# Kernel optimization log

Hardware: AMD Instinct MI355X
Metric: run time of the kernel (lower is better)

Reference implementation:

```python
import jax, jax.numpy as jnp
import numpy as np

B, N, E, H, SD, HID = 4, 512, 1024, 16, 64, 64
D = E // H  # head_dim


def setup_inputs() -> dict:
    key = jax.random.key(0)
    ks = jax.random.split(key, 20)
    s = lambda i, shape, scale: (jax.random.normal(ks[i], shape, dtype=jnp.float32) * scale)
    inp = {
        "query": s(0, (B, N, E), 1.0),
        "key": s(1, (B, N, E), 1.0),
        "value": s(2, (B, N, E), 1.0),
        "state_embeddings": s(3, (B, N, SD), 1.0),
        # projection weights stored [in, out] (transposed vs torch nn.Linear)
        "Wq": s(4, (E, E), E ** -0.5), "bq": jnp.zeros((E,), jnp.float32),
        "Wk": s(5, (E, E), E ** -0.5), "bk": jnp.zeros((E,), jnp.float32),
        "Wv": s(6, (E, E), E ** -0.5), "bv": jnp.zeros((E,), jnp.float32),
        "Wo": s(7, (E, E), E ** -0.5), "bo": jnp.zeros((E,), jnp.float32),
        # CAB compatibility MLP: Linear(2*SD->HID), ReLU, Linear(HID->HID), ReLU, Linear(HID->H)
        "W1": s(8, (2 * SD, HID), (2 * SD) ** -0.5), "b1": jnp.zeros((HID,), jnp.float32),
        "W2": s(9, (HID, HID), HID ** -0.5), "b2": jnp.zeros((HID,), jnp.float32),
        "W3": s(10, (HID, H), HID ** -0.5), "b3": jnp.zeros((H,), jnp.float32),
        "head_temps": jnp.ones((H,), jnp.float32),
    }
    return inp


def reference(query, key, value, state_embeddings,
              Wq, bq, Wk, bk, Wv, bv, Wo, bo,
              W1, b1, W2, b2, W3, b3, head_temps):
    scale = D ** -0.5
    q = (query @ Wq + bq).reshape(B, N, H, D)
    k = (key @ Wk + bk).reshape(B, N, H, D)
    v = (value @ Wv + bv).reshape(B, N, H, D)
    # [B, H, T, S]
    scores = jnp.einsum("bthd,bshd->bhts", q, k) * scale

    # CAB bias: MLP([e_i; e_j]) -> split first layer to avoid materializing pairs
    hi = state_embeddings @ W1[:SD]          # [B, N, HID]
    hj = state_embeddings @ W1[SD:]          # [B, N, HID]
    h = jax.nn.relu(hi[:, :, None, :] + hj[:, None, :, :] + b1)  # [B, N, N, HID]
    h = jax.nn.relu(h @ W2 + b2)
    comp = h @ W3 + b3                        # [B, N, N, H]
    bias = jnp.transpose(comp, (0, 3, 1, 2)) * head_temps[None, :, None, None]
    scores = scores + bias

    attn = jax.nn.softmax(scores, axis=-1)
    out = jnp.einsum("bhts,bshd->bthd", attn, v).reshape(B, N, E)
    return out @ Wo + bo
```

## Files before the change

### kernel.cpp

```cpp
#include <hip/hip_runtime.h>
#include <hip/hip_bf16.h>

typedef unsigned short u16;
typedef short short8 __attribute__((ext_vector_type(8)));
typedef float f32x4 __attribute__((ext_vector_type(4)));
typedef unsigned short u16x4 __attribute__((ext_vector_type(4)));

#define BB 4
#define NS 512
#define EE 1024
#define HH 16
#define DD 64
#define MM (BB*NS)
#define NSQ 2
#define SQW (NS/NSQ)

__device__ __forceinline__ u16 f2bfh(float x) {
  __hip_bfloat16 h = __float2bfloat16(x);
  union { __hip_bfloat16 h; u16 u; } c; c.h = h; return c.u;
}
__device__ __forceinline__ unsigned pkbf(float a, float b) {
  union { __hip_bfloat16 h; u16 u; } ca, cb;
  ca.h = __float2bfloat16(a); cb.h = __float2bfloat16(b);
  return (unsigned)ca.u | ((unsigned)cb.u << 16);
}
union S8 { short8 s; unsigned u[4]; };

__device__ __forceinline__ void gload_lds16(const void* g, void* l) {
  __builtin_amdgcn_global_load_lds(
      (const __attribute__((address_space(1))) unsigned int*)g,
      (__attribute__((address_space(3))) unsigned int*)l, 16, 0, 0);
}


__global__ void cvt_inputs(const float* __restrict__ q, const float* __restrict__ k,
                           const float* __restrict__ v,
                           u16* __restrict__ qb, u16* __restrict__ kb, u16* __restrict__ vb) {
  size_t g = (size_t)blockIdx.x * 256 + threadIdx.x;
  size_t e = g << 3;
  int seg = (int)(e >> 21);
  size_t off = e & ((1u << 21) - 1);
  const float* src = seg == 0 ? q : (seg == 1 ? k : v);
  u16* dst = seg == 0 ? qb : (seg == 1 ? kb : vb);
  float4 f0 = *(const float4*)(src + off);
  float4 f1 = *(const float4*)(src + off + 4);
  S8 r;
  r.u[0] = pkbf(f0.x, f0.y); r.u[1] = pkbf(f0.z, f0.w);
  r.u[2] = pkbf(f1.x, f1.y); r.u[3] = pkbf(f1.z, f1.w);
  *(short8*)(dst + off) = r.s;
}

__global__ void cvt_w(const float* __restrict__ Wq, const float* __restrict__ Wk,
                      const float* __restrict__ Wv, const float* __restrict__ Wo,
                      u16* __restrict__ WqT, u16* __restrict__ WkT,
                      u16* __restrict__ WvT, u16* __restrict__ WoT) {
  int z = blockIdx.z;
  const float* W = z == 0 ? Wq : z == 1 ? Wk : z == 2 ? Wv : Wo;
  u16* WT = z == 0 ? WqT : z == 1 ? WkT : z == 2 ? WvT : WoT;
  int n0 = blockIdx.x << 5, k0 = blockIdx.y << 5;
  __shared__ float tile[32][33];
  int tx = threadIdx.x & 31, ty = threadIdx.x >> 5;
  #pragma unroll
  for (int i = 0; i < 4; ++i) {
    int r = (i << 3) + ty;
    tile[r][tx] = W[(size_t)(k0 + r) * EE + n0 + tx];
  }
  __syncthreads();
  #pragma unroll
  for (int i = 0; i < 4; ++i) {
    int r = (i << 3) + ty;
    WT[(size_t)(n0 + r) * EE + k0 + tx] = f2bfh(tile[tx][r]);
  }
}

__global__ void cvt_w_small(const float* __restrict__ W2, const float* __restrict__ W3,
                            u16* __restrict__ W2T, u16* __restrict__ W3P) {
  int tid = threadIdx.x;
  for (int i = tid; i < 4096; i += 256) {
    int n = i >> 6, k = i & 63;
    W2T[i] = f2bfh(W2[k * 64 + n]);
  }
  for (int i = tid; i < 1024; i += 256) {
    int h = i >> 6, rem = i & 63;
    int k2 = rem >> 5, gg = (rem >> 3) & 3, j = rem & 7;
    int c = (2 * k2 + (j >> 2)) * 16 + gg * 4 + (j & 3);
    W3P[i] = f2bfh(W3[c * 16 + h]);
  }
}


__global__ void hi_hj_kernel(const float* __restrict__ se, const float* __restrict__ W1,
                             const float* __restrict__ b1,
                             float* __restrict__ hi, float* __restrict__ hj) {
  int tid = threadIdx.x;
  int row = blockIdx.x * 4 + (tid >> 6);
  int c = tid & 63;
  float ah = b1[c], aj = 0.f;
  #pragma unroll 8
  for (int k = 0; k < 64; ++k) {
    float s = se[row * 64 + k];
    ah += s * W1[k * 64 + c];
    aj += s * W1[(k + 64) * 64 + c];
  }
  hi[row * 64 + c] = ah;
  hj[row * 64 + c] = aj;
}


template <int MODE>
__device__ __forceinline__ void gemm_body(const u16* __restrict__ A, const u16* __restrict__ Bt,
                                          const float* __restrict__ bias, void* __restrict__ Cout) {
  __shared__ u16 As[128 * 32];
  __shared__ u16 Bs[128 * 32];
  const int tid = threadIdx.x, lane = tid & 63, wave = tid >> 6;
  const int m0 = blockIdx.x * 128, n0 = blockIdx.y * 128;
  const int wr = wave >> 1, wc = wave & 1;

  const f32x4 zero = {0.f, 0.f, 0.f, 0.f};
  f32x4 acc[4][4];
  #pragma unroll
  for (int i = 0; i < 4; ++i)
    #pragma unroll
    for (int j = 0; j < 4; ++j) acc[i][j] = zero;

  const int rA = lane >> 2;
  const int cA = (lane & 3) << 3;

  for (int kt = 0; kt < EE; kt += 32) {
    #pragma unroll
    for (int i = 0; i < 2; ++i) {
      int base = ((i << 2) + wave) << 9;
      int row = (base >> 5) + rA;
      gload_lds16(A  + (size_t)(m0 + row) * EE + kt + cA, As + base);
      gload_lds16(Bt + (size_t)(n0 + row) * EE + kt + cA, Bs + base);
    }
    __syncthreads();
    short8 af[4], bfr[4];
    #pragma unroll
    for (int mf = 0; mf < 4; ++mf) {
      int row = wr * 64 + mf * 16 + (lane & 15);
      af[mf] = *(const short8*)(As + row * 32 + ((lane >> 4) << 3));
    }
    #pragma unroll
    for (int nf = 0; nf < 4; ++nf) {
      int row = wc * 64 + nf * 16 + (lane & 15);
      bfr[nf] = *(const short8*)(Bs + row * 32 + ((lane >> 4) << 3));
    }
    #pragma unroll
    for (int mf = 0; mf < 4; ++mf)
      #pragma unroll
      for (int nf = 0; nf < 4; ++nf)
        acc[mf][nf] = __builtin_amdgcn_mfma_f32_16x16x32_bf16(af[mf], bfr[nf], acc[mf][nf], 0, 0, 0);
    __syncthreads();
  }

  #pragma unroll
  for (int mf = 0; mf < 4; ++mf) {
    #pragma unroll
    for (int nf = 0; nf < 4; ++nf) {
      int col = n0 + wc * 64 + nf * 16 + (lane & 15);
      float bv = bias[col];
      #pragma unroll
      for (int j = 0; j < 4; ++j) {
        int rowm = m0 + wr * 64 + mf * 16 + ((lane >> 4) << 2) + j;
        float v = acc[mf][nf][j] + bv;
        if (MODE == 2) {
          ((float*)Cout)[(size_t)rowm * EE + col] = v;
        } else {
          int bb = rowm >> 9, r = rowm & 511;
          int h = col >> 6, d = col & 63;
          size_t off;
          if (MODE == 0)
            off = ((((size_t)bb * HH + h) * 32 + (r >> 4)) << 10) + ((size_t)(d >> 5) << 9)
                + ((size_t)((((d >> 3) & 3) << 4) + (r & 15)) << 3) + (d & 7);
          else
            off = (((((size_t)bb * HH + h) * 16 + (r >> 5)) * 4 + (d >> 4)) << 9)
                + ((size_t)((((r >> 3) & 3) << 4) + (d & 15)) << 3) + (r & 7);
          ((u16*)Cout)[off] = f2bfh(v);
        }
      }
    }
  }
}

__global__ __launch_bounds__(256, 2) void gemm_proj(
    const u16* __restrict__ qb, const u16* __restrict__ kb, const u16* __restrict__ vb,
    const u16* __restrict__ WqT, const u16* __restrict__ WkT, const u16* __restrict__ WvT,
    const float* __restrict__ bq, const float* __restrict__ bk, const float* __restrict__ bv_,
    u16* __restrict__ qF, u16* __restrict__ kF, u16* __restrict__ vF) {
  int z = blockIdx.z;
  if (z == 0)      gemm_body<0>(qb, WqT, bq, qF);
  else if (z == 1) gemm_body<0>(kb, WkT, bk, kF);
  else             gemm_body<1>(vb, WvT, bv_, vF);
}

__global__ __launch_bounds__(256, 2) void gemm_final(
    const u16* __restrict__ A, const u16* __restrict__ WoT,
    const float* __restrict__ bo, float* __restrict__ C) {
  gemm_body<2>(A, WoT, bo, C);
}


__global__ __launch_bounds__(512, 2) void fused_cab_attn(
    const float* __restrict__ hi, const float* __restrict__ hj,
    const u16* __restrict__ W2T, const u16* __restrict__ W3P,
    const float* __restrict__ b2, const float* __restrict__ b3,
    const float* __restrict__ temps,
    const u16* __restrict__ qF, const u16* __restrict__ kF,
    const u16* __restrict__ vF,
    float* __restrict__ Opart, float* __restrict__ mlpart) {
  const int b = blockIdx.x >> 1, sq = blockIdx.x & 1, tt = blockIdx.y;
  const int t0 = tt << 4;
  const int tid = threadIdx.x, lane = tid & 63, wave = tid >> 6;
  const int g = lane >> 4, sl = lane & 15;

  __shared__ float hi_s[16][80];
  __shared__ float hj_s[32][65];
  __shared__ float b2_s[64], b3_s[16], tp_s[16];
  __shared__ float comp3[16 * 273];
  __shared__ u16 Pl[8][16][40];

  if (tid < 256) {
    int r = tid >> 4, c4 = (tid & 15) << 2;
    float4 hv = *(const float4*)(hi + ((size_t)(b * NS + t0 + r) << 6) + c4);
    *(f32x4*)&hi_s[r][c4] = (f32x4){hv.x, hv.y, hv.z, hv.w};
  } else {
    int ix = tid - 256;
    if (ix < 64) b2_s[ix] = b2[ix];
    else if (ix < 80) b3_s[ix - 64] = b3[ix - 64];
    else if (ix < 96) tp_s[ix - 80] = temps[ix - 80];
  }

  const f32x4 zero = {0.f, 0.f, 0.f, 0.f};
  f32x4 acc[2][4];
  #pragma unroll
  for (int i = 0; i < 2; ++i)
    #pragma unroll
    for (int j = 0; j < 4; ++j) acc[i][j] = zero;
  float m_run[2] = {-3e38f, -3e38f};
  float l_run[2] = {0.f, 0.f};

  for (int pr = 0; pr < 8; ++pr) {
    const int s0p = sq * SQW + (pr << 5);
    __syncthreads();
    {
      int r = tid >> 4, c4 = (tid & 15) << 2;
      float4 a = *(const float4*)(hj + ((size_t)(b * NS + s0p + r) << 6) + c4);
      hj_s[r][c4 + 0] = a.x; hj_s[r][c4 + 1] = a.y;
      hj_s[r][c4 + 2] = a.z; hj_s[r][c4 + 3] = a.w;
    }

    float vsc[2][2][4];

    #pragma unroll
    for (int ta = 0; ta < 2; ++ta) {
      __syncthreads();
      {
        float hjv[2][8];
        #pragma unroll
        for (int kk = 0; kk < 2; ++kk)
          #pragma unroll
          for (int j = 0; j < 8; ++j)
            hjv[kk][j] = hj_s[(ta << 4) + sl][kk * 32 + (g << 3) + j];

        short8 w3f[2];
        #pragma unroll
        for (int k2 = 0; k2 < 2; ++k2)
          w3f[k2] = *(const short8*)(W3P + (sl << 6) + k2 * 32 + (g << 3));

        float b2v[4][4];
        #pragma unroll
        for (int mfc = 0; mfc < 4; ++mfc)
          #pragma unroll
          for (int jj = 0; jj < 4; ++jj)
            b2v[mfc][jj] = b2_s[mfc * 16 + (g << 2) + jj];

        #pragma unroll
        for (int q = 0; q < 2; ++q) {
          int tl = (wave << 1) + q;
          short8 xb[2];
          #pragma unroll
          for (int kk = 0; kk < 2; ++kk) {
            int c0 = kk * 32 + (g << 3);
            f32x4 h0 = *(const f32x4*)&hi_s[tl][c0];
            f32x4 h1 = *(const f32x4*)&hi_s[tl][c0 + 4];
            float x[8];
            #pragma unroll
            for (int j = 0; j < 4; ++j) {
              x[j]     = fmaxf(h0[j] + hjv[kk][j], 0.f);
              x[j + 4] = fmaxf(h1[j] + hjv[kk][j + 4], 0.f);
            }
            S8 r;
            r.u[0] = pkbf(x[0], x[1]); r.u[1] = pkbf(x[2], x[3]);
            r.u[2] = pkbf(x[4], x[5]); r.u[3] = pkbf(x[6], x[7]);
            xb[kk] = r.s;
          }
          f32x4 accY[4];
          #pragma unroll
          for (int i = 0; i < 4; ++i) accY[i] = zero;
          #pragma unroll
          for (int kk = 0; kk < 2; ++kk)
            #pragma unroll
            for (int mfc = 0; mfc < 4; ++mfc) {
              short8 w2 = *(const short8*)(W2T + ((mfc * 16 + sl) << 6) + kk * 32 + (g << 3));
              accY[mfc] = __builtin_amdgcn_mfma_f32_16x16x32_bf16(w2, xb[kk], accY[mfc], 0, 0, 0);
            }
          f32x4 compD = zero;
          #pragma unroll
          for (int k2 = 0; k2 < 2; ++k2) {
            float y[8];
            #pragma unroll
            for (int j = 0; j < 4; ++j) {
              y[j]     = fmaxf(accY[2 * k2][j]     + b2v[2 * k2][j],     0.f);
              y[j + 4] = fmaxf(accY[2 * k2 + 1][j] + b2v[2 * k2 + 1][j], 0.f);
            }
            S8 r;
            r.u[0] = pkbf(y[0], y[1]); r.u[1] = pkbf(y[2], y[3]);
            r.u[2] = pkbf(y[4], y[5]); r.u[3] = pkbf(y[6], y[7]);
            compD = __builtin_amdgcn_mfma_f32_16x16x32_bf16(w3f[k2], r.s, compD, 0, 0, 0);
          }
          #pragma unroll
          for (int jj = 0; jj < 4; ++jj) {
            int h = (g << 2) + jj;
            comp3[h * 273 + sl * 17 + tl] = (compD[jj] + b3_s[h]) * tp_s[h];
          }
        }
      }
      __syncthreads();
      const int s16 = (sq << 4) + (pr << 1) + ta;
      #pragma unroll
      for (int hh = 0; hh < 2; ++hh) {
        int h = (wave << 1) + hh;
        const u16* qb_ = qF + ((((size_t)b * HH + h) * 32 + tt) << 10) + (lane << 3);
        const u16* kb_ = kF + ((((size_t)b * HH + h) * 32 + s16) << 10) + (lane << 3);
        f32x4 accS = zero;
        accS = __builtin_amdgcn_mfma_f32_16x16x32_bf16(*(const short8*)kb_, *(const short8*)qb_, accS, 0, 0, 0);
        accS = __builtin_amdgcn_mfma_f32_16x16x32_bf16(*(const short8*)(kb_ + 512), *(const short8*)(qb_ + 512), accS, 0, 0, 0);
        #pragma unroll
        for (int j = 0; j < 4; ++j)
          vsc[ta][hh][j] = accS[j] * 0.125f + comp3[h * 273 + ((g << 2) + j) * 17 + sl];
      }
    }

    #pragma unroll
    for (int hh = 0; hh < 2; ++hh) {
      int h = (wave << 1) + hh;
      float e[8];
      float mx = -3e38f;
      #pragma unroll
      for (int j = 0; j < 4; ++j)
        mx = fmaxf(mx, fmaxf(vsc[0][hh][j], vsc[1][hh][j]));
      mx = fmaxf(mx, __shfl_xor(mx, 16, 64));
      mx = fmaxf(mx, __shfl_xor(mx, 32, 64));
      float mnew = fmaxf(m_run[hh], mx);
      float c = __expf(m_run[hh] - mnew);
      m_run[hh] = mnew;
      #pragma unroll
      for (int ta = 0; ta < 2; ++ta)
        #pragma unroll
        for (int j = 0; j < 4; ++j)
          e[ta * 4 + j] = __expf(vsc[ta][hh][j] - mnew);
      float ps = ((e[0] + e[1]) + (e[2] + e[3])) + ((e[4] + e[5]) + (e[6] + e[7]));
      ps += __shfl_xor(ps, 16, 64);
      ps += __shfl_xor(ps, 32, 64);
      l_run[hh] = l_run[hh] * c + ps;

      uint2 wA; wA.x = pkbf(e[0], e[1]); wA.y = pkbf(e[2], e[3]);
      uint2 wB; wB.x = pkbf(e[4], e[5]); wB.y = pkbf(e[6], e[7]);
      *(uint2*)&Pl[wave][sl][(g << 2)]      = wA;
      *(uint2*)&Pl[wave][sl][16 + (g << 2)] = wB;
      short8 pf = *(const short8*)&Pl[wave][sl][(g << 3)];

      float cb[4];
      #pragma unroll
      for (int j = 0; j < 4; ++j) cb[j] = __shfl(c, (g << 2) + j, 64);

      const u16* vb0 = vF + (((((size_t)b * HH + h) * 16 + (sq << 3) + pr) * 4) << 9) + (lane << 3);
      #pragma unroll
      for (int nf = 0; nf < 4; ++nf) {
        #pragma unroll
        for (int j = 0; j < 4; ++j) acc[hh][nf][j] *= cb[j];
        short8 vv = *(const short8*)(vb0 + ((size_t)nf << 9));
        acc[hh][nf] = __builtin_amdgcn_mfma_f32_16x16x32_bf16(pf, vv, acc[hh][nf], 0, 0, 0);
      }
    }
  }

  size_t obase = ((size_t)sq * MM + (size_t)b * NS + t0) * EE;
  #pragma unroll
  for (int hh = 0; hh < 2; ++hh) {
    int h = (wave << 1) + hh;
    #pragma unroll
    for (int nf = 0; nf < 4; ++nf)
      #pragma unroll
      for (int j = 0; j < 4; ++j)
        Opart[obase + (size_t)((g << 2) + j) * EE + (h << 6) + nf * 16 + sl] = acc[hh][nf][j];
  }
  if (g == 0) {
    #pragma unroll
    for (int hh = 0; hh < 2; ++hh) {
      int h = (wave << 1) + hh;
      size_t mlb = (((size_t)sq * MM + b * NS + t0 + sl) * HH + h) * 2;
      mlpart[mlb] = m_run[hh];
      mlpart[mlb + 1] = l_run[hh];
    }
  }
}


__global__ void combine_pv(const float* __restrict__ Opart, const float* __restrict__ mlpart,
                           u16* __restrict__ attn_out) {
  int row = blockIdx.x;
  int tid = threadIdx.x;
  int c4 = tid << 2;
  int h = c4 >> 6;
  float m[NSQ], l[NSQ];
  #pragma unroll
  for (int pq = 0; pq < NSQ; ++pq) {
    size_t mb = (((size_t)pq * MM + row) * HH + h) * 2;
    m[pq] = mlpart[mb]; l[pq] = mlpart[mb + 1];
  }
  float M = m[0];
  #pragma unroll
  for (int pq = 1; pq < NSQ; ++pq) M = fmaxf(M, m[pq]);
  float den = 0.f;
  f32x4 num = {0.f, 0.f, 0.f, 0.f};
  #pragma unroll
  for (int pq = 0; pq < NSQ; ++pq) {
    float w = __expf(m[pq] - M);
    den += w * l[pq];
    f32x4 o = *(const f32x4*)(Opart + ((size_t)pq * MM + row) * EE + c4);
    #pragma unroll
    for (int i = 0; i < 4; ++i) num[i] += w * o[i];
  }
  float r = 1.0f / den;
  u16x4 out;
  #pragma unroll
  for (int i = 0; i < 4; ++i) out[i] = f2bfh(num[i] * r);
  *(u16x4*)(attn_out + (size_t)row * EE + c4) = out;
}


extern "C" void kernel_launch(void* const* d_in, const int* in_sizes, int n_in,
                              void* d_out, int out_size, void* d_ws, size_t ws_size,
                              hipStream_t stream) {
  const float* query = (const float*)d_in[0];
  const float* key   = (const float*)d_in[1];
  const float* value = (const float*)d_in[2];
  const float* se    = (const float*)d_in[3];
  const float* Wq = (const float*)d_in[4];  const float* bq = (const float*)d_in[5];
  const float* Wk = (const float*)d_in[6];  const float* bk = (const float*)d_in[7];
  const float* Wv = (const float*)d_in[8];  const float* bv = (const float*)d_in[9];
  const float* Wo = (const float*)d_in[10]; const float* bo = (const float*)d_in[11];
  const float* W1 = (const float*)d_in[12]; const float* b1 = (const float*)d_in[13];
  const float* W2 = (const float*)d_in[14]; const float* b2 = (const float*)d_in[15];
  const float* W3 = (const float*)d_in[16]; const float* b3 = (const float*)d_in[17];
  const float* temps = (const float*)d_in[18];

  char* p = (char*)d_ws;
  auto alloc = [&](size_t bytes) { char* r = p; p += (bytes + 255) & ~(size_t)255; return r; };
  u16* qb  = (u16*)alloc((size_t)MM * EE * 2);
  u16* kb  = (u16*)alloc((size_t)MM * EE * 2);
  u16* vb  = (u16*)alloc((size_t)MM * EE * 2);
  u16* WqT = (u16*)alloc((size_t)EE * EE * 2);
  u16* WkT = (u16*)alloc((size_t)EE * EE * 2);
  u16* WvT = (u16*)alloc((size_t)EE * EE * 2);
  u16* WoT = (u16*)alloc((size_t)EE * EE * 2);
  u16* W2T = (u16*)alloc(4096 * 2);
  u16* W3P = (u16*)alloc(1024 * 2);
  u16* qF  = (u16*)alloc((size_t)MM * EE * 2);
  u16* kF  = (u16*)alloc((size_t)MM * EE * 2);
  u16* vF  = (u16*)alloc((size_t)MM * EE * 2);
  float* hi = (float*)alloc((size_t)MM * 64 * 4);
  float* hj = (float*)alloc((size_t)MM * 64 * 4);
  float* Opart = (float*)alloc((size_t)NSQ * MM * EE * 4);
  float* mlpart = (float*)alloc((size_t)NSQ * MM * HH * 2 * 4);
  u16* attn_out = (u16*)alloc((size_t)MM * EE * 2);
  (void)ws_size; (void)in_sizes; (void)n_in; (void)out_size;

  cvt_inputs<<<3072, 256, 0, stream>>>(query, key, value, qb, kb, vb);
  cvt_w<<<dim3(32, 32, 4), 256, 0, stream>>>(Wq, Wk, Wv, Wo, WqT, WkT, WvT, WoT);
  cvt_w_small<<<1, 256, 0, stream>>>(W2, W3, W2T, W3P);
  hi_hj_kernel<<<512, 256, 0, stream>>>(se, W1, b1, hi, hj);
  gemm_proj<<<dim3(16, 8, 3), 256, 0, stream>>>(qb, kb, vb, WqT, WkT, WvT, bq, bk, bv, qF, kF, vF);
  fused_cab_attn<<<dim3(8, 32, 1), 512, 0, stream>>>(hi, hj, W2T, W3P, b2, b3, temps,
                                                     qF, kF, vF, Opart, mlpart);
  combine_pv<<<MM, 256, 0, stream>>>(Opart, mlpart, attn_out);
  gemm_final<<<dim3(16, 8, 1), 256, 0, stream>>>(attn_out, WoT, bo, (float*)d_out);
}
```

Before: 122.7 us.

## Split attention key range four ways and hoist per-block constants out of loop

Increases the key-range split from 2 to 4, doubling the grid of the fused CAB+attention kernel to 512 blocks for better CU occupancy. Moves W3, b2, b3, temps and Q fragments into registers loaded once per block instead of per iteration. Double-buffers comp3 so both 16-key sub-tiles are computed before one barrier, cutting syncs per iteration. The trade-offs are more register pressure, larger partial output buffers, and more work for the combine kernel. The combine kernel (not shown) must handle NSQ=4 through the macro.

```diff
diff --git a/kernel.cpp b/kernel.cpp
--- a/kernel.cpp
+++ b/kernel.cpp
@@ -12,7 +12,7 @@
 #define HH 16
 #define DD 64
 #define MM (BB*NS)
-#define NSQ 2
+#define NSQ 4
 #define SQW (NS/NSQ)
 
 __device__ __forceinline__ u16 f2bfh(float x) {
@@ -209,26 +209,48 @@
     const u16* __restrict__ qF, const u16* __restrict__ kF,
     const u16* __restrict__ vF,
     float* __restrict__ Opart, float* __restrict__ mlpart) {
-  const int b = blockIdx.x >> 1, sq = blockIdx.x & 1, tt = blockIdx.y;
+  const int b = blockIdx.x >> 2, sq = blockIdx.x & 3, tt = blockIdx.y;
   const int t0 = tt << 4;
   const int tid = threadIdx.x, lane = tid & 63, wave = tid >> 6;
   const int g = lane >> 4, sl = lane & 15;
 
   __shared__ float hi_s[16][80];
   __shared__ float hj_s[32][65];
-  __shared__ float b2_s[64], b3_s[16], tp_s[16];
-  __shared__ float comp3[16 * 273];
+  __shared__ float comp3[2][16 * 273];
   __shared__ u16 Pl[8][16][40];
 
   if (tid < 256) {
     int r = tid >> 4, c4 = (tid & 15) << 2;
     float4 hv = *(const float4*)(hi + ((size_t)(b * NS + t0 + r) << 6) + c4);
     *(f32x4*)&hi_s[r][c4] = (f32x4){hv.x, hv.y, hv.z, hv.w};
-  } else {
-    int ix = tid - 256;
-    if (ix < 64) b2_s[ix] = b2[ix];
-    else if (ix < 80) b3_s[ix - 64] = b3[ix - 64];
-    else if (ix < 96) tp_s[ix - 80] = temps[ix - 80];
+  }
+
+  short8 w3f[2];
+  #pragma unroll
+  for (int k2 = 0; k2 < 2; ++k2)
+    w3f[k2] = *(const short8*)(W3P + (sl << 6) + k2 * 32 + (g << 3));
+
+  float b2v[4][4];
+  #pragma unroll
+  for (int mfc = 0; mfc < 4; ++mfc)
+    #pragma unroll
+    for (int jj = 0; jj < 4; ++jj)
+      b2v[mfc][jj] = b2[mfc * 16 + (g << 2) + jj];
+
+  float b3v[4], tpv[4];
+  #pragma unroll
+  for (int jj = 0; jj < 4; ++jj) {
+    b3v[jj] = b3[(g << 2) + jj];
+    tpv[jj] = temps[(g << 2) + jj];
+  }
+
+  short8 qf[2][2];
+  #pragma unroll
+  for (int hh = 0; hh < 2; ++hh) {
+    int h = (wave << 1) + hh;
+    const u16* qb_ = qF + ((((size_t)b * HH + h) * 32 + tt) << 10) + (lane << 3);
+    qf[hh][0] = *(const short8*)qb_;
+    qf[hh][1] = *(const short8*)(qb_ + 512);
   }
 
   const f32x4 zero = {0.f, 0.f, 0.f, 0.f};
@@ -240,7 +262,7 @@
   float m_run[2] = {-3e38f, -3e38f};
   float l_run[2] = {0.f, 0.f};
 
-  for (int pr = 0; pr < 8; ++pr) {
+  for (int pr = 0; pr < NSQ; ++pr) {
     const int s0p = sq * SQW + (pr << 5);
     __syncthreads();
     {
@@ -249,96 +271,84 @@
       hj_s[r][c4 + 0] = a.x; hj_s[r][c4 + 1] = a.y;
       hj_s[r][c4 + 2] = a.z; hj_s[r][c4 + 3] = a.w;
     }
-
-    float vsc[2][2][4];
+    __syncthreads();
 
     #pragma unroll
     for (int ta = 0; ta < 2; ++ta) {
-      __syncthreads();
-      {
-        float hjv[2][8];
+      float hjv[2][8];
+      #pragma unroll
+      for (int kk = 0; kk < 2; ++kk)
+        #pragma unroll
+        for (int j = 0; j < 8; ++j)
+          hjv[kk][j] = hj_s[(ta << 4) + sl][kk * 32 + (g << 3) + j];
+
+      #pragma unroll
+      for (int q = 0; q < 2; ++q) {
+        int tl = (wave << 1) + q;
+        short8 xb[2];
+        #pragma unroll
+        for (int kk = 0; kk < 2; ++kk) {
+          int c0 = kk * 32 + (g << 3);
+          f32x4 h0 = *(const f32x4*)&hi_s[tl][c0];
+          f32x4 h1 = *(const f32x4*)&hi_s[tl][c0 + 4];
+          float x[8];
+          #pragma unroll
+          for (int j = 0; j < 4; ++j) {
+            x[j]     = fmaxf(h0[j] + hjv[kk][j], 0.f);
+            x[j + 4] = fmaxf(h1[j] + hjv[kk][j + 4], 0.f);
+          }
+          S8 r;
+          r.u[0] = pkbf(x[0], x[1]); r.u[1] = pkbf(x[2], x[3]);
+          r.u[2] = pkbf(x[4], x[5]); r.u[3] = pkbf(x[6], x[7]);
+          xb[kk] = r.s;
+        }
+        f32x4 accY[4];
+        #pragma unroll
+        for (int i = 0; i < 4; ++i) accY[i] = zero;
         #pragma unroll
         for (int kk = 0; kk < 2; ++kk)
           #pragma unroll
-          for (int j = 0; j < 8; ++j)
-            hjv[kk][j] = hj_s[(ta << 4) + sl][kk * 32 + (g << 3) + j];
-
-        short8 w3f[2];
-        #pragma unroll
-        for (int k2 = 0; k2 < 2; ++k2)
-          w3f[k2] = *(const short8*)(W3P + (sl << 6) + k2 * 32 + (g << 3));
-
-        float b2v[4][4];
-        #pragma unroll
-        for (int mfc = 0; mfc < 4; ++mfc)
+          for (int mfc = 0; mfc < 4; ++mfc) {
+            short8 w2 = *(const short8*)(W2T + ((mfc * 16 + sl) << 6) + kk * 32 + (g << 3));
+            accY[mfc] = __builtin_amdgcn_mfma_f32_16x16x32_bf16(w2, xb[kk], accY[mfc], 0, 0, 0);
+          }
+        f32x4 compD = zero;
+        #pragma unroll
+        for (int k2 = 0; k2 < 2; ++k2) {
+          float y[8];
           #pragma unroll
-          for (int jj = 0; jj < 4; ++jj)
-            b2v[mfc][jj] = b2_s[mfc * 16 + (g << 2) + jj];
-
-        #pragma unroll
-        for (int q = 0; q < 2; ++q) {
-          int tl = (wave << 1) + q;
-          short8 xb[2];
-          #pragma unroll
-          for (int kk = 0; kk < 2; ++kk) {
-            int c0 = kk * 32 + (g << 3);
-            f32x4 h0 = *(const f32x4*)&hi_s[tl][c0];
-            f32x4 h1 = *(const f32x4*)&hi_s[tl][c0 + 4];
-            float x[8];
-            #pragma unroll
-            for (int j = 0; j < 4; ++j) {
-              x[j]     = fmaxf(h0[j] + hjv[kk][j], 0.f);
-              x[j + 4] = fmaxf(h1[j] + hjv[kk][j + 4], 0.f);
-            }
-            S8 r;
-            r.u[0] = pkbf(x[0], x[1]); r.u[1] = pkbf(x[2], x[3]);
-            r.u[2] = pkbf(x[4], x[5]); r.u[3] = pkbf(x[6], x[7]);
-            xb[kk] = r.s;
+          for (int j = 0; j < 4; ++j) {
+            y[j]     = fmaxf(accY[2 * k2][j]     + b2v[2 * k2][j],     0.f);
+            y[j + 4] = fmaxf(accY[2 * k2 + 1][j] + b2v[2 * k2 + 1][j], 0.f);
           }
-          f32x4 accY[4];
-          #pragma unroll
-          for (int i = 0; i < 4; ++i) accY[i] = zero;
-          #pragma unroll
-          for (int kk = 0; kk < 2; ++kk)
-            #pragma unroll
-            for (int mfc = 0; mfc < 4; ++mfc) {
-              short8 w2 = *(const short8*)(W2T + ((mfc * 16 + sl) << 6) + kk * 32 + (g << 3));
-              accY[mfc] = __builtin_amdgcn_mfma_f32_16x16x32_bf16(w2, xb[kk], accY[mfc], 0, 0, 0);
-            }
-          f32x4 compD = zero;
-          #pragma unroll
-          for (int k2 = 0; k2 < 2; ++k2) {
-            float y[8];
-            #pragma unroll
-            for (int j = 0; j < 4; ++j) {
-              y[j]     = fmaxf(accY[2 * k2][j]     + b2v[2 * k2][j],     0.f);
-              y[j + 4] = fmaxf(accY[2 * k2 + 1][j] + b2v[2 * k2 + 1][j], 0.f);
-            }
-            S8 r;
-            r.u[0] = pkbf(y[0], y[1]); r.u[1] = pkbf(y[2], y[3]);
-            r.u[2] = pkbf(y[4], y[5]); r.u[3] = pkbf(y[6], y[7]);
-            compD = __builtin_amdgcn_mfma_f32_16x16x32_bf16(w3f[k2], r.s, compD, 0, 0, 0);
-          }
-          #pragma unroll
-          for (int jj = 0; jj < 4; ++jj) {
-            int h = (g << 2) + jj;
-            comp3[h * 273 + sl * 17 + tl] = (compD[jj] + b3_s[h]) * tp_s[h];
-          }
+          S8 r;
+          r.u[0] = pkbf(y[0], y[1]); r.u[1] = pkbf(y[2], y[3]);
+          r.u[2] = pkbf(y[4], y[5]); r.u[3] = pkbf(y[6], y[7]);
+          compD = __builtin_amdgcn_mfma_f32_16x16x32_bf16(w3f[k2], r.s, compD, 0, 0, 0);
+        }
+        #pragma unroll
+        for (int jj = 0; jj < 4; ++jj) {
+          int h = (g << 2) + jj;
+          comp3[ta][h * 273 + sl * 17 + tl] = (compD[jj] + b3v[jj]) * tpv[jj];
         }
       }
-      __syncthreads();
-      const int s16 = (sq << 4) + (pr << 1) + ta;
+    }
+    __syncthreads();
+
+    float vsc[2][2][4];
+    #pragma unroll
+    for (int ta = 0; ta < 2; ++ta) {
+      const int s16 = (sq << 3) + (pr << 1) + ta;
       #pragma unroll
       for (int hh = 0; hh < 2; ++hh) {
         int h = (wave << 1) + hh;
-        const u16* qb_ = qF + ((((size_t)b * HH + h) * 32 + tt) << 10) + (lane << 3);
         const u16* kb_ = kF + ((((size_t)b * HH + h) * 32 + s16) << 10) + (lane << 3);
         f32x4 accS = zero;
-        accS = __builtin_amdgcn_mfma_f32_16x16x32_bf16(*(const short8*)kb_, *(const short8*)qb_, accS, 0, 0, 0);
-        accS = __builtin_amdgcn_mfma_f32_16x16x32_bf16(*(const short8*)(kb_ + 512), *(const short8*)(qb_ + 512), accS, 0, 0, 0);
+        accS = __builtin_amdgcn_mfma_f32_16x16x32_bf16(*(const short8*)kb_, qf[hh][0], accS, 0, 0, 0);
+        accS = __builtin_amdgcn_mfma_f32_16x16x32_bf16(*(const short8*)(kb_ + 512), qf[hh][1], accS, 0, 0, 0);
         #pragma unroll
         for (int j = 0; j < 4; ++j)
-          vsc[ta][hh][j] = accS[j] * 0.125f + comp3[h * 273 + ((g << 2) + j) * 17 + sl];
+          vsc[ta][hh][j] = accS[j] * 0.125f + comp3[ta][h * 273 + ((g << 2) + j) * 17 + sl];
       }
     }
 
@@ -375,7 +385,7 @@
       #pragma unroll
       for (int j = 0; j < 4; ++j) cb[j] = __shfl(c, (g << 2) + j, 64);
 
-      const u16* vb0 = vF + (((((size_t)b * HH + h) * 16 + (sq << 3) + pr) * 4) << 9) + (lane << 3);
+      const u16* vb0 = vF + (((((size_t)b * HH + h) * 16 + (sq << 2) + pr) * 4) << 9) + (lane << 3);
       #pragma unroll
       for (int nf = 0; nf < 4; ++nf) {
         #pragma unroll
@@ -483,8 +493,8 @@
   cvt_w_small<<<1, 256, 0, stream>>>(W2, W3, W2T, W3P);
   hi_hj_kernel<<<512, 256, 0, stream>>>(se, W1, b1, hi, hj);
   gemm_proj<<<dim3(16, 8, 3), 256, 0, stream>>>(qb, kb, vb, WqT, WkT, WvT, bq, bk, bv, qF, kF, vF);
-  fused_cab_attn<<<dim3(8, 32, 1), 512, 0, stream>>>(hi, hj, W2T, W3P, b2, b3, temps,
-                                                     qF, kF, vF, Opart, mlpart);
+  fused_cab_attn<<<dim3(16, 32, 1), 512, 0, stream>>>(hi, hj, W2T, W3P, b2, b3, temps,
+                                                      qF, kF, vF, Opart, mlpart);
   combine_pv<<<MM, 256, 0, stream>>>(Opart, mlpart, attn_out);
   gemm_final<<<dim3(16, 8, 1), 256, 0, stream>>>(attn_out, WoT, bo, (float*)d_out);
 }
```

New measurement: 136.0 us. 1.11x slower.

## Double-buffer hj tiles in fused attention and merge small weight conversion into cvt_w

Applied to the files above, without the earlier changes.

The fused CAB-attention kernel now double-buffers the hj tile in shared memory. The next tile is loaded into registers early in each iteration and written to the alternate buffer after the MLP stage, which hides global-load latency and drops one barrier per outer iteration. Separately, the single-block W2/W3 conversion kernel is folded into cvt_w as an extra z-slice, saving one kernel launch. The cost is about 8 KB more LDS and more live registers, which could reduce occupancy under launch_bounds(512,2).

```diff
diff --git a/kernel.cpp b/kernel.cpp
--- a/kernel.cpp
+++ b/kernel.cpp
@@ -52,9 +52,26 @@
 
 __global__ void cvt_w(const float* __restrict__ Wq, const float* __restrict__ Wk,
                       const float* __restrict__ Wv, const float* __restrict__ Wo,
+                      const float* __restrict__ W2, const float* __restrict__ W3,
                       u16* __restrict__ WqT, u16* __restrict__ WkT,
-                      u16* __restrict__ WvT, u16* __restrict__ WoT) {
+                      u16* __restrict__ WvT, u16* __restrict__ WoT,
+                      u16* __restrict__ W2T, u16* __restrict__ W3P) {
   int z = blockIdx.z;
+  if (z == 4) {
+    if (blockIdx.x || blockIdx.y) return;
+    int tid = threadIdx.x;
+    for (int i = tid; i < 4096; i += 256) {
+      int n = i >> 6, k = i & 63;
+      W2T[i] = f2bfh(W2[k * 64 + n]);
+    }
+    for (int i = tid; i < 1024; i += 256) {
+      int h = i >> 6, rem = i & 63;
+      int k2 = rem >> 5, gg = (rem >> 3) & 3, j = rem & 7;
+      int c = (2 * k2 + (j >> 2)) * 16 + gg * 4 + (j & 3);
+      W3P[i] = f2bfh(W3[c * 16 + h]);
+    }
+    return;
+  }
   const float* W = z == 0 ? Wq : z == 1 ? Wk : z == 2 ? Wv : Wo;
   u16* WT = z == 0 ? WqT : z == 1 ? WkT : z == 2 ? WvT : WoT;
   int n0 = blockIdx.x << 5, k0 = blockIdx.y << 5;
@@ -70,21 +87,6 @@
   for (int i = 0; i < 4; ++i) {
     int r = (i << 3) + ty;
     WT[(size_t)(n0 + r) * EE + k0 + tx] = f2bfh(tile[tx][r]);
-  }
-}
-
-__global__ void cvt_w_small(const float* __restrict__ W2, const float* __restrict__ W3,
-                            u16* __restrict__ W2T, u16* __restrict__ W3P) {
-  int tid = threadIdx.x;
-  for (int i = tid; i < 4096; i += 256) {
-    int n = i >> 6, k = i & 63;
-    W2T[i] = f2bfh(W2[k * 64 + n]);
-  }
-  for (int i = tid; i < 1024; i += 256) {
-    int h = i >> 6, rem = i & 63;
-    int k2 = rem >> 5, gg = (rem >> 3) & 3, j = rem & 7;
-    int c = (2 * k2 + (j >> 2)) * 16 + gg * 4 + (j & 3);
-    W3P[i] = f2bfh(W3[c * 16 + h]);
   }
 }
 
@@ -215,7 +217,7 @@
   const int g = lane >> 4, sl = lane & 15;
 
   __shared__ float hi_s[16][80];
-  __shared__ float hj_s[32][65];
+  __shared__ float hj_s[2][32][65];
   __shared__ float b2_s[64], b3_s[16], tp_s[16];
   __shared__ float comp3[16 * 273];
   __shared__ u16 Pl[8][16][40];
@@ -231,6 +233,13 @@
     else if (ix < 96) tp_s[ix - 80] = temps[ix - 80];
   }
 
+  const int hr = tid >> 4, hc4 = (tid & 15) << 2;
+  {
+    float4 a = *(const float4*)(hj + ((size_t)(b * NS + sq * SQW + hr) << 6) + hc4);
+    hj_s[0][hr][hc4 + 0] = a.x; hj_s[0][hr][hc4 + 1] = a.y;
+    hj_s[0][hr][hc4 + 2] = a.z; hj_s[0][hr][hc4 + 3] = a.w;
+  }
+
   const f32x4 zero = {0.f, 0.f, 0.f, 0.f};
   f32x4 acc[2][4];
   #pragma unroll
@@ -240,28 +249,28 @@
   float m_run[2] = {-3e38f, -3e38f};
   float l_run[2] = {0.f, 0.f};
 
+  int cur = 0;
   for (int pr = 0; pr < 8; ++pr) {
     const int s0p = sq * SQW + (pr << 5);
     __syncthreads();
-    {
-      int r = tid >> 4, c4 = (tid & 15) << 2;
-      float4 a = *(const float4*)(hj + ((size_t)(b * NS + s0p + r) << 6) + c4);
-      hj_s[r][c4 + 0] = a.x; hj_s[r][c4 + 1] = a.y;
-      hj_s[r][c4 + 2] = a.z; hj_s[r][c4 + 3] = a.w;
-    }
+
+    float4 hjnx;
+    const bool have = (pr + 1) < 8;
+    if (have)
+      hjnx = *(const float4*)(hj + ((size_t)(b * NS + s0p + 32 + hr) << 6) + hc4);
 
     float vsc[2][2][4];
 
     #pragma unroll
     for (int ta = 0; ta < 2; ++ta) {
-      __syncthreads();
+      if (ta) __syncthreads();
       {
         float hjv[2][8];
         #pragma unroll
         for (int kk = 0; kk < 2; ++kk)
           #pragma unroll
           for (int j = 0; j < 8; ++j)
-            hjv[kk][j] = hj_s[(ta << 4) + sl][kk * 32 + (g << 3) + j];
+            hjv[kk][j] = hj_s[cur][(ta << 4) + sl][kk * 32 + (g << 3) + j];
 
         short8 w3f[2];
         #pragma unroll
@@ -342,6 +351,11 @@
       }
     }
 
+    if (have) {
+      hj_s[cur ^ 1][hr][hc4 + 0] = hjnx.x; hj_s[cur ^ 1][hr][hc4 + 1] = hjnx.y;
+      hj_s[cur ^ 1][hr][hc4 + 2] = hjnx.z; hj_s[cur ^ 1][hr][hc4 + 3] = hjnx.w;
+    }
+
     #pragma unroll
     for (int hh = 0; hh < 2; ++hh) {
       int h = (wave << 1) + hh;
@@ -384,6 +398,7 @@
         acc[hh][nf] = __builtin_amdgcn_mfma_f32_16x16x32_bf16(pf, vv, acc[hh][nf], 0, 0, 0);
       }
     }
+    cur ^= 1;
   }
 
   size_t obase = ((size_t)sq * MM + (size_t)b * NS + t0) * EE;
@@ -479,8 +494,8 @@
   (void)ws_size; (void)in_sizes; (void)n_in; (void)out_size;
 
   cvt_inputs<<<3072, 256, 0, stream>>>(query, key, value, qb, kb, vb);
-  cvt_w<<<dim3(32, 32, 4), 256, 0, stream>>>(Wq, Wk, Wv, Wo, WqT, WkT, WvT, WoT);
-  cvt_w_small<<<1, 256, 0, stream>>>(W2, W3, W2T, W3P);
+  cvt_w<<<dim3(32, 32, 5), 256, 0, stream>>>(Wq, Wk, Wv, Wo, W2, W3,
+                                             WqT, WkT, WvT, WoT, W2T, W3P);
   hi_hj_kernel<<<512, 256, 0, stream>>>(se, W1, b1, hi, hj);
   gemm_proj<<<dim3(16, 8, 3), 256, 0, stream>>>(qb, kb, vb, WqT, WkT, WvT, bq, bk, bv, qF, kF, vF);
   fused_cab_attn<<<dim3(8, 32, 1), 512, 0, stream>>>(hi, hj, W2T, W3P, b2, b3, temps,
```

After: 121.6 us. No clear change (-0.9%).
